# Performance work log

Measured on AMD Instinct MI355X. Metric: run time of the kernel, lower is better.

Reference implementation:

```python
import jax, jax.numpy as jnp
import numpy as np
import math

IMG_COUNT = 5      # total_length = id_length + 1
NUM_TOKENS = 576   # (768//32)**2, the is_1024_resolution branch
CHANNELS = 1280
N_SEL = 288        # sa32 * NUM_TOKENS
HEADS = 20


def setup_inputs() -> dict:
    key = jax.random.key(0)
    ks = jax.random.split(key, 7)
    hidden_states = jax.random.normal(ks[0], (2 * IMG_COUNT, NUM_TOKENS, CHANNELS), dtype=jnp.float32)
    scale = 0.02
    Wq = jax.random.normal(ks[1], (CHANNELS, CHANNELS), dtype=jnp.float32) * scale
    Wk = jax.random.normal(ks[2], (CHANNELS, CHANNELS), dtype=jnp.float32) * scale
    Wv = jax.random.normal(ks[3], (CHANNELS, CHANNELS), dtype=jnp.float32) * scale
    Wo = jax.random.normal(ks[4], (CHANNELS, CHANNELS), dtype=jnp.float32) * scale
    bo = jnp.zeros((CHANNELS,), dtype=jnp.float32)
    # per-image random spatial token subsets (cal_attn_indice_xl_effcient_memory)
    indices = jax.random.randint(ks[5], (IMG_COUNT, N_SEL), 0, NUM_TOKENS, dtype=jnp.int64)
    return {"hidden_states": hidden_states, "Wq": Wq, "Wk": Wk, "Wv": Wv,
            "Wo": Wo, "bo": bo, "indices": indices, "heads": HEADS}


def _sdpa_block(q_in, kv_in, Wq, Wk, Wv, Wo, bo, heads):
    """Faithful __call2__: linear q/k/v, multi-head SDPA, output projection."""
    B, Tq, C = q_in.shape
    Tk = kv_in.shape[1]
    hd = C // heads
    q = (q_in @ Wq.T).reshape(B, Tq, heads, hd).transpose(0, 2, 1, 3)   # [B,H,Tq,hd]
    k = (kv_in @ Wk.T).reshape(B, Tk, heads, hd).transpose(0, 2, 1, 3)  # [B,H,Tk,hd]
    v = (kv_in @ Wv.T).reshape(B, Tk, heads, hd).transpose(0, 2, 1, 3)
    scale = 1.0 / math.sqrt(hd)
    scores = jnp.einsum('bhqd,bhkd->bhqk', q, k) * scale
    probs = jax.nn.softmax(scores, axis=-1)
    o = jnp.einsum('bhqk,bhkd->bhqd', probs, v)
    o = o.transpose(0, 2, 1, 3).reshape(B, Tq, C)
    return o @ Wo.T + bo


def reference(hidden_states, Wq, Wk, Wv, Wo, bo, indices, heads):
    B, T, C = hidden_states.shape
    P = indices.shape[0]          # img_count
    hs = hidden_states.reshape(2, P, T, C)
    # gathered[p] = hs[:, p, indices[p], :] -> [2, P, n_sel, C]
    gathered = hs[:, jnp.arange(P)[:, None], indices, :]
    outs = []
    for i in range(P):            # small fixed loop over images (structurally distinct KV banks)
        cur = hs[:, i]            # [2, T, C]
        others = jnp.concatenate([gathered[:, p] for p in range(P) if p != i], axis=1)
        enc = jnp.concatenate([others, cur], axis=1)  # [2, (P-1)*n_sel + T, C]
        outs.append(_sdpa_block(cur, enc, Wq, Wk, Wv, Wo, bo, heads))
    return jnp.stack(outs, axis=1).reshape(B, T, C)
```

## Files before the change

### kernel.cpp

```cpp
#include <hip/hip_runtime.h>

typedef __bf16 bf16_t;
typedef __attribute__((ext_vector_type(4))) __bf16 bf16x4;
typedef __attribute__((ext_vector_type(8))) __bf16 bf16x8;
typedef __attribute__((ext_vector_type(4))) float f32x4;

#define MFMA_BF16(a, b, c) __builtin_amdgcn_mfma_f32_16x16x32_bf16((a), (b), (c), 0, 0, 0)

namespace {

constexpr int PIMG  = 5;
constexpr int TTOK  = 576;
constexpr int CCH   = 1280;
constexpr int NSEL  = 288;
constexpr int NH    = 20;
constexpr int ROWS  = 2 * PIMG * TTOK;
constexpr int TKEYS = 4 * NSEL + TTOK;
constexpr int KT_TILES = TKEYS / 64;
constexpr size_t NXE = (size_t)ROWS * CCH;
constexpr size_t NWE = (size_t)CCH * CCH;

__device__ __forceinline__ bf16x8 cvt8(const float* p) {
  const float4 f0 = *(const float4*)p;
  const float4 f1 = *(const float4*)(p + 4);
  bf16x8 r;
  r[0] = (bf16_t)f0.x; r[1] = (bf16_t)f0.y; r[2] = (bf16_t)f0.z; r[3] = (bf16_t)f0.w;
  r[4] = (bf16_t)f1.x; r[5] = (bf16_t)f1.y; r[6] = (bf16_t)f1.z; r[7] = (bf16_t)f1.w;
  return r;
}

__global__ __launch_bounds__(256) void cvt_kernel(
    const float* __restrict__ X, const float* __restrict__ W0, const float* __restrict__ W1,
    const float* __restrict__ W2, const float* __restrict__ W3,
    bf16_t* __restrict__ Xb, bf16_t* __restrict__ Wb0, bf16_t* __restrict__ Wb1,
    bf16_t* __restrict__ Wb2, bf16_t* __restrict__ Wb3) {
  const int y = blockIdx.y;
  const float* src = y == 0 ? X : (y == 1 ? W0 : (y == 2 ? W1 : (y == 3 ? W2 : W3)));
  bf16_t* dst = y == 0 ? Xb : (y == 1 ? Wb0 : (y == 2 ? Wb1 : (y == 3 ? Wb2 : Wb3)));
  const size_t n = y == 0 ? NXE : NWE;
  const size_t idx = ((size_t)blockIdx.x * 256 + threadIdx.x) * 8;
  if (idx < n) *(bf16x8*)&dst[idx] = cvt8(&src[idx]);
}

template <bool BIAS, typename CT>
__device__ __forceinline__ void gemm_nt_body(const bf16_t* __restrict__ A,
                                             const bf16_t* __restrict__ B,
                                             const float* __restrict__ bias,
                                             CT* __restrict__ C,
                                             int bm, int bn, float scale) {
  constexpr int LDT = 72;
  __shared__ bf16_t As[128 * LDT];
  __shared__ bf16_t Bs[128 * LDT];

  const int tid  = threadIdx.x;
  const int lane = tid & 63;
  const int wave = tid >> 6;
  const int quad = lane >> 4;
  const int l16  = lane & 15;
  const int wr   = (wave >> 1) * 64;
  const int wc   = (wave & 1) * 64;
  const int m0   = bm * 128;
  const int n0   = bn * 128;
  const int srow = tid >> 3;
  const int scol = (tid & 7) * 8;

  bf16x8 pa[4], pb[4];
  auto loadAB = [&](int k0) {
#pragma unroll
    for (int p = 0; p < 4; ++p) {
      pa[p] = *(const bf16x8*)&A[(size_t)(m0 + srow + 32 * p) * CCH + k0 + scol];
      pb[p] = *(const bf16x8*)&B[(size_t)(n0 + srow + 32 * p) * CCH + k0 + scol];
    }
  };
  loadAB(0);

  f32x4 acc[4][4];
#pragma unroll
  for (int i = 0; i < 4; ++i)
#pragma unroll
    for (int j = 0; j < 4; ++j) acc[i][j] = (f32x4){0.f, 0.f, 0.f, 0.f};

  for (int it = 0; it < CCH / 64; ++it) {
#pragma unroll
    for (int p = 0; p < 4; ++p) {
      *(bf16x8*)&As[(srow + 32 * p) * LDT + scol] = pa[p];
      *(bf16x8*)&Bs[(srow + 32 * p) * LDT + scol] = pb[p];
    }
    __syncthreads();
    if (it < CCH / 64 - 1) loadAB((it + 1) * 64);
#pragma unroll
    for (int ks = 0; ks < 2; ++ks) {
      bf16x8 af[4], bfr[4];
#pragma unroll
      for (int i = 0; i < 4; ++i)
        af[i] = *(const bf16x8*)&As[(wr + 16 * i + l16) * LDT + ks * 32 + quad * 8];
#pragma unroll
      for (int j = 0; j < 4; ++j)
        bfr[j] = *(const bf16x8*)&Bs[(wc + 16 * j + l16) * LDT + ks * 32 + quad * 8];
#pragma unroll
      for (int i = 0; i < 4; ++i)
#pragma unroll
        for (int j = 0; j < 4; ++j)
          acc[i][j] = MFMA_BF16(af[i], bfr[j], acc[i][j]);
    }
    if (it < CCH / 64 - 1) __syncthreads();
  }

#pragma unroll
  for (int j = 0; j < 4; ++j) {
    const int col = n0 + wc + 16 * j + l16;
    const float bv = BIAS ? bias[col] : 0.f;
#pragma unroll
    for (int i = 0; i < 4; ++i) {
#pragma unroll
      for (int r = 0; r < 4; ++r) {
        const int row = m0 + wr + 16 * i + quad * 4 + r;
        const float val = acc[i][j][r] * scale + bv;
        if constexpr (sizeof(CT) == 2)
          C[(size_t)row * CCH + col] = (CT)val;
        else
          C[(size_t)row * CCH + col] = val;
      }
    }
  }
}

__global__ __launch_bounds__(256, 3) void qkv_gemm_kernel(
    const bf16_t* __restrict__ Xb,
    const bf16_t* __restrict__ Wqb, const bf16_t* __restrict__ Wkb, const bf16_t* __restrict__ Wvb,
    bf16_t* __restrict__ Qf, bf16_t* __restrict__ Kf, bf16_t* __restrict__ Vf) {
  const bf16_t* W = blockIdx.z == 0 ? Wqb : (blockIdx.z == 1 ? Wkb : Wvb);
  bf16_t* O = blockIdx.z == 0 ? Qf : (blockIdx.z == 1 ? Kf : Vf);
  const float scl = blockIdx.z == 0 ? 0.125f : 1.0f;
  gemm_nt_body<false, bf16_t>(Xb, W, nullptr, O, blockIdx.x, blockIdx.y, scl);
}

__global__ __launch_bounds__(256, 3) void out_gemm_kernel(
    const bf16_t* __restrict__ Of, const bf16_t* __restrict__ Wob,
    const float* __restrict__ bo, float* __restrict__ out) {
  gemm_nt_body<true, float>(Of, Wob, bo, out, blockIdx.x, blockIdx.y, 1.0f);
}

__global__ __launch_bounds__(256, 4) void attn_kernel(
    const bf16_t* __restrict__ Qf, const bf16_t* __restrict__ Kf, const bf16_t* __restrict__ Vf,
    const int* __restrict__ indices, bf16_t* __restrict__ Ofull) {
  __shared__ unsigned short kvrow[TKEYS];
  __shared__ bf16_t Vts[64 * 64];
  __shared__ bf16_t Ps[64 * 72];

  const int tid  = threadIdx.x;
  const int lane = tid & 63;
  const int wave = tid >> 6;
  const int quad = lane >> 4;
  const int l16  = lane & 15;

  const int b   = blockIdx.x;
  const int xcd = b & 7;
  const int t   = b >> 3;
  const int gi  = t / 9;
  const int qt  = t - gi * 9;
  const int g   = xcd + 8 * gi;
  const int h   = g % NH;
  const int si  = g / NH;
  const int s   = si / PIMG;
  const int ii  = si % PIMG;

  const int r0 = si * TTOK + qt * 64;
  const int hc = h * 64;

  bf16x8 aq[4][2];
#pragma unroll
  for (int n = 0; n < 4; ++n)
#pragma unroll
    for (int h2 = 0; h2 < 2; ++h2)
      aq[n][h2] = *(const bf16x8*)&Qf[(size_t)(r0 + 16 * n + l16) * CCH + hc + quad * 8 + 32 * h2];

  for (int j = tid; j < TKEYS; j += 256) {
    int row;
    if (j < 4 * NSEL) {
      const int jp = j / NSEL;
      const int jj = j - jp * NSEL;
      const int p  = jp + (jp >= ii ? 1 : 0);
      row = (s * PIMG + p) * TTOK + indices[p * NSEL + jj];
    } else {
      row = si * TTOK + (j - 4 * NSEL);
    }
    kvrow[j] = (unsigned short)row;
  }
  __syncthreads();

  const int jrow = tid >> 3;
  const int cdim = (tid & 7) * 8;

  bf16x8 kf0, kf1, vv0, vv1;
  bf16x8 nk0, nk1, nv0, nv1;
  auto load_tile = [&](int kt, bf16x8& a, bf16x8& b, bf16x8& c, bf16x8& d) {
    const int krow = kvrow[kt * 64 + 16 * wave + l16];
    a = *(const bf16x8*)&Kf[(size_t)krow * CCH + hc + quad * 8];
    b = *(const bf16x8*)&Kf[(size_t)krow * CCH + hc + quad * 8 + 32];
    const int ra = kvrow[kt * 64 + jrow];
    const int rb = kvrow[kt * 64 + jrow + 32];
    c = *(const bf16x8*)&Vf[(size_t)ra * CCH + hc + cdim];
    d = *(const bf16x8*)&Vf[(size_t)rb * CCH + hc + cdim];
  };
  load_tile(0, kf0, kf1, vv0, vv1);

  float l_part[4] = {0.f, 0.f, 0.f, 0.f};
  f32x4 oacc[4];
#pragma unroll
  for (int n = 0; n < 4; ++n) oacc[n] = (f32x4){0.f, 0.f, 0.f, 0.f};

  for (int kt = 0; kt < KT_TILES; ++kt) {
    const int cb0 = jrow ^ cdim;
    const int cb1 = (jrow + 32) ^ cdim;
#pragma unroll
    for (int x = 0; x < 8; ++x) {
      Vts[(cdim + x) * 64 + cb0] = vv0[x];
      Vts[(cdim + x) * 64 + cb1] = vv1[x];
    }
    __syncthreads();
    if (kt < KT_TILES - 1) load_tile(kt + 1, nk0, nk1, nv0, nv1);

    f32x4 sacc[4];
#pragma unroll
    for (int n = 0; n < 4; ++n) {
      f32x4 z = (f32x4){0.f, 0.f, 0.f, 0.f};
      z = MFMA_BF16(kf0, aq[n][0], z);
      z = MFMA_BF16(kf1, aq[n][1], z);
      sacc[n] = z;
    }

#pragma unroll
    for (int n = 0; n < 4; ++n) {
      bf16x4 pb;
      float sum = 0.f;
#pragma unroll
      for (int r = 0; r < 4; ++r) {
        const float pv = __expf(sacc[n][r]);
        pb[r] = (bf16_t)pv;
        sum += pv;
      }
      l_part[n] += sum;
      *(bf16x4*)&Ps[(16 * n + l16) * 72 + 16 * wave + 4 * quad] = pb;
    }
    __syncthreads();

    const bf16x8 vf0 = *(const bf16x8*)&Vts[(16 * wave + l16) * 64 + ((quad * 8) ^ ((16 * wave + l16) & 56))];
    const bf16x8 vf1 = *(const bf16x8*)&Vts[(16 * wave + l16) * 64 + ((quad * 8 + 32) ^ ((16 * wave + l16) & 56))];
#pragma unroll
    for (int n = 0; n < 4; ++n) {
      const bf16x8 pf0 = *(const bf16x8*)&Ps[(16 * n + l16) * 72 + quad * 8];
      const bf16x8 pf1 = *(const bf16x8*)&Ps[(16 * n + l16) * 72 + quad * 8 + 32];
      oacc[n] = MFMA_BF16(pf0, vf0, oacc[n]);
      oacc[n] = MFMA_BF16(pf1, vf1, oacc[n]);
    }
    __syncthreads();

    kf0 = nk0; kf1 = nk1; vv0 = nv0; vv1 = nv1;
  }

  float* lred = (float*)Ps;
  float* linv = (float*)Vts;
#pragma unroll
  for (int n = 0; n < 4; ++n)
    lred[(16 * n + l16) * 16 + 4 * wave + quad] = l_part[n];
  __syncthreads();
  if (tid < 64) {
    float tt = 0.f;
#pragma unroll
    for (int i = 0; i < 16; ++i) tt += lred[tid * 16 + i];
    linv[tid] = 1.f / tt;
  }
  __syncthreads();
#pragma unroll
  for (int n = 0; n < 4; ++n) {
#pragma unroll
    for (int r = 0; r < 4; ++r) {
      const int qloc = 16 * n + 4 * quad + r;
      Ofull[(size_t)(r0 + qloc) * CCH + hc + 16 * wave + l16] =
          (bf16_t)(oacc[n][r] * linv[qloc]);
    }
  }
}

}

extern "C" void kernel_launch(void* const* d_in, const int* in_sizes, int n_in,
                              void* d_out, int out_size, void* d_ws, size_t ws_size,
                              hipStream_t stream) {
  const float* hs = (const float*)d_in[0];
  const float* Wq = (const float*)d_in[1];
  const float* Wk = (const float*)d_in[2];
  const float* Wv = (const float*)d_in[3];
  const float* Wo = (const float*)d_in[4];
  const float* bo = (const float*)d_in[5];
  const int* indices = (const int*)d_in[6];
  float* out = (float*)d_out;

  bf16_t* Qf  = (bf16_t*)d_ws;
  bf16_t* Kf  = Qf + NXE;
  bf16_t* Vf  = Kf + NXE;
  bf16_t* Xb  = Vf + NXE;
  bf16_t* Of  = Xb;
  bf16_t* Wqb = Xb + NXE;
  bf16_t* Wkb = Wqb + NWE;
  bf16_t* Wvb = Wkb + NWE;
  bf16_t* Wob = Wvb + NWE;

  dim3 g0((NXE + 2047) / 2048, 5);
  cvt_kernel<<<g0, dim3(256), 0, stream>>>(hs, Wq, Wk, Wv, Wo, Xb, Wqb, Wkb, Wvb, Wob);

  dim3 g1(ROWS / 128, CCH / 128, 3);
  qkv_gemm_kernel<<<g1, dim3(256), 0, stream>>>(Xb, Wqb, Wkb, Wvb, Qf, Kf, Vf);

  attn_kernel<<<dim3(1800), dim3(256), 0, stream>>>(Qf, Kf, Vf, indices, Of);

  dim3 g3(ROWS / 128, CCH / 128, 1);
  out_gemm_kernel<<<g3, dim3(256), 0, stream>>>(Of, Wob, bo, out);
}
```

Measured before the change: 316.3 us.

## Enlarge attention query tile to 144 rows with Q staged in LDS

```diff
diff --git a/kernel.cpp b/kernel.cpp
--- a/kernel.cpp
+++ b/kernel.cpp
@@ -19,6 +19,10 @@
 constexpr int KT_TILES = TKEYS / 64;
 constexpr size_t NXE = (size_t)ROWS * CCH;
 constexpr size_t NWE = (size_t)CCH * CCH;
+
+constexpr int QB   = 144;
+constexpr int NFR  = QB / 16;
+constexpr int NQT  = TTOK / QB;
 
 __device__ __forceinline__ bf16x8 cvt8(const float* p) {
   const float4 f0 = *(const float4*)p;
@@ -141,12 +145,13 @@
   gemm_nt_body<true, float>(Of, Wob, bo, out, blockIdx.x, blockIdx.y, 1.0f);
 }
 
-__global__ __launch_bounds__(256, 4) void attn_kernel(
+__global__ __launch_bounds__(256, 3) void attn_kernel(
     const bf16_t* __restrict__ Qf, const bf16_t* __restrict__ Kf, const bf16_t* __restrict__ Vf,
     const int* __restrict__ indices, bf16_t* __restrict__ Ofull) {
   __shared__ unsigned short kvrow[TKEYS];
+  __shared__ bf16_t Qs[QB * 72];
   __shared__ bf16_t Vts[64 * 64];
-  __shared__ bf16_t Ps[64 * 72];
+  __shared__ bf16_t Ps[QB * 72];
 
   const int tid  = threadIdx.x;
   const int lane = tid & 63;
@@ -157,23 +162,22 @@
   const int b   = blockIdx.x;
   const int xcd = b & 7;
   const int t   = b >> 3;
-  const int gi  = t / 9;
-  const int qt  = t - gi * 9;
+  const int gi  = t >> 2;
+  const int qt  = t & 3;
   const int g   = xcd + 8 * gi;
   const int h   = g % NH;
   const int si  = g / NH;
   const int s   = si / PIMG;
   const int ii  = si % PIMG;
 
-  const int r0 = si * TTOK + qt * 64;
+  const int r0 = si * TTOK + qt * QB;
   const int hc = h * 64;
 
-  bf16x8 aq[4][2];
-#pragma unroll
-  for (int n = 0; n < 4; ++n)
-#pragma unroll
-    for (int h2 = 0; h2 < 2; ++h2)
-      aq[n][h2] = *(const bf16x8*)&Qf[(size_t)(r0 + 16 * n + l16) * CCH + hc + quad * 8 + 32 * h2];
+  for (int idx = tid; idx < QB * 8; idx += 256) {
+    const int row = idx >> 3;
+    const int c8  = (idx & 7) * 8;
+    *(bf16x8*)&Qs[row * 72 + c8] = *(const bf16x8*)&Qf[(size_t)(r0 + row) * CCH + hc + c8];
+  }
 
   for (int j = tid; j < TKEYS; j += 256) {
     int row;
@@ -194,10 +198,10 @@
 
   bf16x8 kf0, kf1, vv0, vv1;
   bf16x8 nk0, nk1, nv0, nv1;
-  auto load_tile = [&](int kt, bf16x8& a, bf16x8& b, bf16x8& c, bf16x8& d) {
+  auto load_tile = [&](int kt, bf16x8& a, bf16x8& b2, bf16x8& c, bf16x8& d) {
     const int krow = kvrow[kt * 64 + 16 * wave + l16];
-    a = *(const bf16x8*)&Kf[(size_t)krow * CCH + hc + quad * 8];
-    b = *(const bf16x8*)&Kf[(size_t)krow * CCH + hc + quad * 8 + 32];
+    a  = *(const bf16x8*)&Kf[(size_t)krow * CCH + hc + quad * 8];
+    b2 = *(const bf16x8*)&Kf[(size_t)krow * CCH + hc + quad * 8 + 32];
     const int ra = kvrow[kt * 64 + jrow];
     const int rb = kvrow[kt * 64 + jrow + 32];
     c = *(const bf16x8*)&Vf[(size_t)ra * CCH + hc + cdim];
@@ -205,50 +209,51 @@
   };
   load_tile(0, kf0, kf1, vv0, vv1);
 
-  float l_part[4] = {0.f, 0.f, 0.f, 0.f};
-  f32x4 oacc[4];
-#pragma unroll
-  for (int n = 0; n < 4; ++n) oacc[n] = (f32x4){0.f, 0.f, 0.f, 0.f};
+  float l_part[NFR];
+  f32x4 oacc[NFR];
+#pragma unroll
+  for (int n = 0; n < NFR; ++n) {
+    l_part[n] = 0.f;
+    oacc[n] = (f32x4){0.f, 0.f, 0.f, 0.f};
+  }
+
+  const int cb0 = jrow ^ cdim;
+  const int cb1 = (jrow + 32) ^ cdim;
 
   for (int kt = 0; kt < KT_TILES; ++kt) {
-    const int cb0 = jrow ^ cdim;
-    const int cb1 = (jrow + 32) ^ cdim;
+    if (kt < KT_TILES - 1) load_tile(kt + 1, nk0, nk1, nv0, nv1);
+
 #pragma unroll
     for (int x = 0; x < 8; ++x) {
       Vts[(cdim + x) * 64 + cb0] = vv0[x];
       Vts[(cdim + x) * 64 + cb1] = vv1[x];
     }
-    __syncthreads();
-    if (kt < KT_TILES - 1) load_tile(kt + 1, nk0, nk1, nv0, nv1);
-
-    f32x4 sacc[4];
-#pragma unroll
-    for (int n = 0; n < 4; ++n) {
+
+#pragma unroll
+    for (int n = 0; n < NFR; ++n) {
+      const bf16x8 af0 = *(const bf16x8*)&Qs[(16 * n + l16) * 72 + quad * 8];
+      const bf16x8 af1 = *(const bf16x8*)&Qs[(16 * n + l16) * 72 + quad * 8 + 32];
       f32x4 z = (f32x4){0.f, 0.f, 0.f, 0.f};
-      z = MFMA_BF16(kf0, aq[n][0], z);
-      z = MFMA_BF16(kf1, aq[n][1], z);
-      sacc[n] = z;
-    }
-
-#pragma unroll
-    for (int n = 0; n < 4; ++n) {
+      z = MFMA_BF16(kf0, af0, z);
+      z = MFMA_BF16(kf1, af1, z);
       bf16x4 pb;
       float sum = 0.f;
 #pragma unroll
       for (int r = 0; r < 4; ++r) {
-        const float pv = __expf(sacc[n][r]);
+        const float pv = __expf(z[r]);
         pb[r] = (bf16_t)pv;
         sum += pv;
       }
       l_part[n] += sum;
       *(bf16x4*)&Ps[(16 * n + l16) * 72 + 16 * wave + 4 * quad] = pb;
     }
+
     __syncthreads();
 
     const bf16x8 vf0 = *(const bf16x8*)&Vts[(16 * wave + l16) * 64 + ((quad * 8) ^ ((16 * wave + l16) & 56))];
     const bf16x8 vf1 = *(const bf16x8*)&Vts[(16 * wave + l16) * 64 + ((quad * 8 + 32) ^ ((16 * wave + l16) & 56))];
 #pragma unroll
-    for (int n = 0; n < 4; ++n) {
+    for (int n = 0; n < NFR; ++n) {
       const bf16x8 pf0 = *(const bf16x8*)&Ps[(16 * n + l16) * 72 + quad * 8];
       const bf16x8 pf1 = *(const bf16x8*)&Ps[(16 * n + l16) * 72 + quad * 8 + 32];
       oacc[n] = MFMA_BF16(pf0, vf0, oacc[n]);
@@ -262,10 +267,10 @@
   float* lred = (float*)Ps;
   float* linv = (float*)Vts;
 #pragma unroll
-  for (int n = 0; n < 4; ++n)
+  for (int n = 0; n < NFR; ++n)
     lred[(16 * n + l16) * 16 + 4 * wave + quad] = l_part[n];
   __syncthreads();
-  if (tid < 64) {
+  if (tid < QB) {
     float tt = 0.f;
 #pragma unroll
     for (int i = 0; i < 16; ++i) tt += lred[tid * 16 + i];
@@ -273,7 +278,7 @@
   }
   __syncthreads();
 #pragma unroll
-  for (int n = 0; n < 4; ++n) {
+  for (int n = 0; n < NFR; ++n) {
 #pragma unroll
     for (int r = 0; r < 4; ++r) {
       const int qloc = 16 * n + 4 * quad + r;
@@ -313,7 +318,7 @@
   dim3 g1(ROWS / 128, CCH / 128, 3);
   qkv_gemm_kernel<<<g1, dim3(256), 0, stream>>>(Xb, Wqb, Wkb, Wvb, Qf, Kf, Vf);
 
-  attn_kernel<<<dim3(1800), dim3(256), 0, stream>>>(Qf, Kf, Vf, indices, Of);
+  attn_kernel<<<dim3(200 * NQT), dim3(256), 0, stream>>>(Qf, Kf, Vf, indices, Of);
 
   dim3 g3(ROWS / 128, CCH / 128, 1);
   out_gemm_kernel<<<g3, dim3(256), 0, stream>>>(Of, Wob, bo, out);
```

New measurement: 325.9 us. +3.1%, slower.

## Restructure attention kernel to two waves keeping P in registers with double-buffered V

Applied to the files above, without the earlier changes.

```diff
diff --git a/kernel.cpp b/kernel.cpp
--- a/kernel.cpp
+++ b/kernel.cpp
@@ -141,12 +141,11 @@
   gemm_nt_body<true, float>(Of, Wob, bo, out, blockIdx.x, blockIdx.y, 1.0f);
 }
 
-__global__ __launch_bounds__(256, 4) void attn_kernel(
+__global__ __launch_bounds__(128, 2) void attn_kernel(
     const bf16_t* __restrict__ Qf, const bf16_t* __restrict__ Kf, const bf16_t* __restrict__ Vf,
     const int* __restrict__ indices, bf16_t* __restrict__ Ofull) {
   __shared__ unsigned short kvrow[TKEYS];
-  __shared__ bf16_t Vts[64 * 64];
-  __shared__ bf16_t Ps[64 * 72];
+  __shared__ __align__(16) bf16_t Vts[2][64 * 64];
 
   const int tid  = threadIdx.x;
   const int lane = tid & 63;
@@ -175,7 +174,7 @@
     for (int h2 = 0; h2 < 2; ++h2)
       aq[n][h2] = *(const bf16x8*)&Qf[(size_t)(r0 + 16 * n + l16) * CCH + hc + quad * 8 + 32 * h2];
 
-  for (int j = tid; j < TKEYS; j += 256) {
+  for (int j = tid; j < TKEYS; j += 128) {
     int row;
     if (j < 4 * NSEL) {
       const int jp = j / NSEL;
@@ -189,97 +188,138 @@
   }
   __syncthreads();
 
-  const int jrow = tid >> 3;
-  const int cdim = (tid & 7) * 8;
-
-  bf16x8 kf0, kf1, vv0, vv1;
-  bf16x8 nk0, nk1, nv0, nv1;
-  auto load_tile = [&](int kt, bf16x8& a, bf16x8& b, bf16x8& c, bf16x8& d) {
-    const int krow = kvrow[kt * 64 + 16 * wave + l16];
-    a = *(const bf16x8*)&Kf[(size_t)krow * CCH + hc + quad * 8];
-    b = *(const bf16x8*)&Kf[(size_t)krow * CCH + hc + quad * 8 + 32];
-    const int ra = kvrow[kt * 64 + jrow];
-    const int rb = kvrow[kt * 64 + jrow + 32];
-    c = *(const bf16x8*)&Vf[(size_t)ra * CCH + hc + cdim];
-    d = *(const bf16x8*)&Vf[(size_t)rb * CCH + hc + cdim];
-  };
-  load_tile(0, kf0, kf1, vv0, vv1);
+  const int kidx = 32 * wave + ((l16 >> 2) << 3) + (l16 & 3);
+
+  const int va = tid >> 3;
+  const int vc = (tid & 7) * 8;
+
+  bf16x8 kq[2][2], kn[2][2], vs[4], vn[4];
+#pragma unroll
+  for (int kg = 0; kg < 2; ++kg) {
+    const int krow = kvrow[kidx + 4 * kg];
+    kq[kg][0] = *(const bf16x8*)&Kf[(size_t)krow * CCH + hc + quad * 8];
+    kq[kg][1] = *(const bf16x8*)&Kf[(size_t)krow * CCH + hc + quad * 8 + 32];
+  }
+#pragma unroll
+  for (int e = 0; e < 4; ++e)
+    vs[e] = *(const bf16x8*)&Vf[(size_t)kvrow[4 * va + e] * CCH + hc + vc];
 
   float l_part[4] = {0.f, 0.f, 0.f, 0.f};
-  f32x4 oacc[4];
-#pragma unroll
-  for (int n = 0; n < 4; ++n) oacc[n] = (f32x4){0.f, 0.f, 0.f, 0.f};
+  f32x4 oacc[4][4];
+#pragma unroll
+  for (int n = 0; n < 4; ++n)
+#pragma unroll
+    for (int dg = 0; dg < 4; ++dg) oacc[n][dg] = (f32x4){0.f, 0.f, 0.f, 0.f};
 
   for (int kt = 0; kt < KT_TILES; ++kt) {
-    const int cb0 = jrow ^ cdim;
-    const int cb1 = (jrow + 32) ^ cdim;
-#pragma unroll
-    for (int x = 0; x < 8; ++x) {
-      Vts[(cdim + x) * 64 + cb0] = vv0[x];
-      Vts[(cdim + x) * 64 + cb1] = vv1[x];
-    }
+    {
+      unsigned int* V32 = (unsigned int*)&Vts[kt & 1][0];
+      const unsigned short* q0 = (const unsigned short*)&vs[0];
+      const unsigned short* q1 = (const unsigned short*)&vs[1];
+      const unsigned short* q2 = (const unsigned short*)&vs[2];
+      const unsigned short* q3 = (const unsigned short*)&vs[3];
+#pragma unroll
+      for (int x = 0; x < 8; ++x) {
+        const int sx = (vc >> 1) ^ (x << 2);
+        V32[(vc + x) * 32 + ((2 * va) ^ sx)]     = (unsigned int)q0[x] | ((unsigned int)q1[x] << 16);
+        V32[(vc + x) * 32 + ((2 * va + 1) ^ sx)] = (unsigned int)q2[x] | ((unsigned int)q3[x] << 16);
+      }
+    }
+
+    if (kt + 1 < KT_TILES) {
+      const int kb = (kt + 1) * 64;
+#pragma unroll
+      for (int kg = 0; kg < 2; ++kg) {
+        const int krow = kvrow[kb + kidx + 4 * kg];
+        kn[kg][0] = *(const bf16x8*)&Kf[(size_t)krow * CCH + hc + quad * 8];
+        kn[kg][1] = *(const bf16x8*)&Kf[(size_t)krow * CCH + hc + quad * 8 + 32];
+      }
+#pragma unroll
+      for (int e = 0; e < 4; ++e)
+        vn[e] = *(const bf16x8*)&Vf[(size_t)kvrow[kb + 4 * va + e] * CCH + hc + vc];
+    }
+
+    bf16x8 pa[4];
+#pragma unroll
+    for (int kg = 0; kg < 2; ++kg) {
+#pragma unroll
+      for (int n = 0; n < 4; ++n) {
+        f32x4 z = (f32x4){0.f, 0.f, 0.f, 0.f};
+        z = MFMA_BF16(kq[kg][0], aq[n][0], z);
+        z = MFMA_BF16(kq[kg][1], aq[n][1], z);
+#pragma unroll
+        for (int r = 0; r < 4; ++r) {
+          const float pv = __expf(z[r]);
+          l_part[n] += pv;
+          pa[n][4 * kg + r] = (bf16_t)pv;
+        }
+      }
+    }
+
     __syncthreads();
-    if (kt < KT_TILES - 1) load_tile(kt + 1, nk0, nk1, nv0, nv1);
-
-    f32x4 sacc[4];
-#pragma unroll
-    for (int n = 0; n < 4; ++n) {
-      f32x4 z = (f32x4){0.f, 0.f, 0.f, 0.f};
-      z = MFMA_BF16(kf0, aq[n][0], z);
-      z = MFMA_BF16(kf1, aq[n][1], z);
-      sacc[n] = z;
-    }
-
-#pragma unroll
-    for (int n = 0; n < 4; ++n) {
-      bf16x4 pb;
-      float sum = 0.f;
-#pragma unroll
-      for (int r = 0; r < 4; ++r) {
-        const float pv = __expf(sacc[n][r]);
-        pb[r] = (bf16_t)pv;
-        sum += pv;
-      }
-      l_part[n] += sum;
-      *(bf16x4*)&Ps[(16 * n + l16) * 72 + 16 * wave + 4 * quad] = pb;
-    }
-    __syncthreads();
-
-    const bf16x8 vf0 = *(const bf16x8*)&Vts[(16 * wave + l16) * 64 + ((quad * 8) ^ ((16 * wave + l16) & 56))];
-    const bf16x8 vf1 = *(const bf16x8*)&Vts[(16 * wave + l16) * 64 + ((quad * 8 + 32) ^ ((16 * wave + l16) & 56))];
-#pragma unroll
-    for (int n = 0; n < 4; ++n) {
-      const bf16x8 pf0 = *(const bf16x8*)&Ps[(16 * n + l16) * 72 + quad * 8];
-      const bf16x8 pf1 = *(const bf16x8*)&Ps[(16 * n + l16) * 72 + quad * 8 + 32];
-      oacc[n] = MFMA_BF16(pf0, vf0, oacc[n]);
-      oacc[n] = MFMA_BF16(pf1, vf1, oacc[n]);
-    }
-    __syncthreads();
-
-    kf0 = nk0; kf1 = nk1; vv0 = nv0; vv1 = nv1;
-  }
-
-  float* lred = (float*)Ps;
-  float* linv = (float*)Vts;
+
+    const bf16_t* __restrict__ Vb = &Vts[kt & 1][0];
+#pragma unroll
+    for (int dg = 0; dg < 4; ++dg) {
+      const int d  = 16 * dg + l16;
+      const int sw = (d & 56) ^ ((d & 7) << 3);
+      const bf16x8 vf = *(const bf16x8*)&Vb[d * 64 + ((32 * wave + 8 * quad) ^ sw)];
+#pragma unroll
+      for (int n = 0; n < 4; ++n)
+        oacc[n][dg] = MFMA_BF16(pa[n], vf, oacc[n][dg]);
+    }
+
+#pragma unroll
+    for (int kg = 0; kg < 2; ++kg) {
+      kq[kg][0] = kn[kg][0];
+      kq[kg][1] = kn[kg][1];
+    }
+#pragma unroll
+    for (int e = 0; e < 4; ++e) vs[e] = vn[e];
+  }
+
+  __syncthreads();
+
+  float* lred = (float*)kvrow;
+  float* linv = lred + 512;
 #pragma unroll
   for (int n = 0; n < 4; ++n)
-    lred[(16 * n + l16) * 16 + 4 * wave + quad] = l_part[n];
+    lred[(16 * n + l16) * 8 + 4 * wave + quad] = l_part[n];
   __syncthreads();
   if (tid < 64) {
     float tt = 0.f;
 #pragma unroll
-    for (int i = 0; i < 16; ++i) tt += lred[tid * 16 + i];
+    for (int i = 0; i < 8; ++i) tt += lred[tid * 8 + i];
     linv[tid] = 1.f / tt;
   }
   __syncthreads();
-#pragma unroll
-  for (int n = 0; n < 4; ++n) {
-#pragma unroll
-    for (int r = 0; r < 4; ++r) {
-      const int qloc = 16 * n + 4 * quad + r;
-      Ofull[(size_t)(r0 + qloc) * CCH + hc + 16 * wave + l16] =
-          (bf16_t)(oacc[n][r] * linv[qloc]);
-    }
+
+  float* Osc = (float*)&Vts[0][0];
+  if (wave == 0) {
+#pragma unroll
+    for (int n = 0; n < 4; ++n)
+#pragma unroll
+      for (int r = 0; r < 4; ++r) {
+        const int q = 16 * n + 4 * quad + r;
+#pragma unroll
+        for (int dg = 0; dg < 4; ++dg)
+          Osc[q * 64 + 16 * dg + l16] = oacc[n][dg][r];
+      }
+  }
+  __syncthreads();
+  if (wave == 1) {
+#pragma unroll
+    for (int n = 0; n < 4; ++n)
+#pragma unroll
+      for (int r = 0; r < 4; ++r) {
+        const int q   = 16 * n + 4 * quad + r;
+        const float inv = linv[q];
+#pragma unroll
+        for (int dg = 0; dg < 4; ++dg) {
+          const float val = (Osc[q * 64 + 16 * dg + l16] + oacc[n][dg][r]) * inv;
+          Ofull[(size_t)(r0 + q) * CCH + hc + 16 * dg + l16] = (bf16_t)val;
+        }
+      }
   }
 }
 
@@ -313,7 +353,7 @@
   dim3 g1(ROWS / 128, CCH / 128, 3);
   qkv_gemm_kernel<<<g1, dim3(256), 0, stream>>>(Xb, Wqb, Wkb, Wvb, Qf, Kf, Vf);
 
-  attn_kernel<<<dim3(1800), dim3(256), 0, stream>>>(Qf, Kf, Vf, indices, Of);
+  attn_kernel<<<dim3(1800), dim3(128), 0, stream>>>(Qf, Kf, Vf, indices, Of);
 
   dim3 g3(ROWS / 128, CCH / 128, 1);
   out_gemm_kernel<<<g3, dim3(256), 0, stream>>>(Of, Wob, bo, out);
```

New measurement: 303.0 us. 1.04x faster.
